# Kernel tuning notes

Measured on AMD Instinct MI355X. Metric: run time of the kernel, lower is better.

The kernel has to match this reference:

```python
import jax, jax.numpy as jnp
import numpy as np
import math

STEM = 64
TOK = 128
RADIUS = 0.16
K = 32


def sinusoidal_pos_emb_3d(x, dim):
    # x: [..., 3] -> [..., dim]; dim/3 channels per axis (half sin, half cos)
    per_axis = dim // 3
    half = per_axis // 2
    scale = math.log(10000.0) / (half - 1)
    freqs = jnp.exp(-scale * jnp.arange(half, dtype=x.dtype))  # [half]
    ang = x[..., :, None] * freqs  # [..., 3, half]
    emb = jnp.concatenate([jnp.sin(ang), jnp.cos(ang)], axis=-1)  # [..., 3, per_axis]
    return emb.reshape(*x.shape[:-1], dim)


def query_ball_point(radius, nsample, xyz):
    # xyz: [B, N, 3] -> idx [B, N, nsample] int32
    B, N, _ = xyz.shape
    d2 = jnp.sum((xyz[:, :, None, :] - xyz[:, None, :, :]) ** 2, axis=-1)  # [B,N,N]
    cand = jnp.where(d2 <= radius * radius, jnp.arange(N, dtype=jnp.int32)[None, None, :], N)
    idx = jnp.sort(cand, axis=-1)[..., :nsample]  # first nsample in-ball indices
    first = idx[..., :1]  # self is always in-ball (d=0), so first is valid
    return jnp.where(idx == N, first, idx)


def index_points(points, idx):
    # points [B,N,C], idx [B,S,K] -> [B,S,K,C]
    return jax.vmap(lambda p, i: p[i])(points, idx)


def point_mlp(x, W, b, activate):
    y = x @ W + b
    return jax.nn.relu(y) if activate else y


def setup_inputs() -> dict:
    key = jax.random.key(0)
    ks = jax.random.split(key, 10)
    B, N = 2, 4096
    xyz = jax.random.uniform(ks[0], (B, N, 3), dtype=jnp.float32)
    point_feature = jax.random.normal(ks[1], (B, N, STEM), dtype=jnp.float32)
    c_in = STEM + 3 + 24 + 96  # 187
    def lin(k, i, o):
        s = 1.0 / np.sqrt(i)
        return jax.random.uniform(k, (i, o), jnp.float32, -s, s)
    W1 = lin(ks[2], c_in, TOK); b1 = jnp.zeros((TOK,), jnp.float32)
    W2 = lin(ks[3], TOK, TOK); b2 = jnp.zeros((TOK,), jnp.float32)
    W3 = lin(ks[4], TOK, TOK); b3 = jnp.zeros((TOK,), jnp.float32)
    W4 = lin(ks[5], TOK, TOK); b4 = jnp.zeros((TOK,), jnp.float32)
    return {"xyz": xyz, "point_feature": point_feature,
            "W1": W1, "b1": b1, "W2": W2, "b2": b2,
            "W3": W3, "b3": b3, "W4": W4, "b4": b4}


def reference(xyz, point_feature, W1, b1, W2, b2, W3, b3, W4, b4):
    idx = query_ball_point(RADIUS, K, xyz)                 # [B,N,K]
    grouped_xyz = index_points(xyz, idx)                   # [B,N,K,3]
    grouped_feature = index_points(point_feature, idx)     # [B,N,K,STEM]
    relative_xyz = grouped_xyz - xyz[:, :, None, :]        # [B,N,K,3]
    rel_pe = sinusoidal_pos_emb_3d(relative_xyz, 24)       # [B,N,K,24]
    abs_pe = sinusoidal_pos_emb_3d(xyz, 96)                # [B,N,96]
    abs_pe = jnp.broadcast_to(abs_pe[:, :, None, :], (*idx.shape, 96))
    grouped_input = jnp.concatenate(
        [grouped_feature, relative_xyz, rel_pe, abs_pe], axis=-1)  # [B,N,K,187]
    h = point_mlp(grouped_input, W1, b1, True)
    h = point_mlp(h, W2, b2, False)                        # [B,N,K,TOK]
    scene_point_feature = jnp.max(h, axis=2)               # [B,N,TOK]
    g = jnp.max(scene_point_feature, axis=1, keepdims=True)  # [B,1,TOK]
    g = point_mlp(g, W3, b3, True)
    return point_mlp(g, W4, b4, False)                     # [B,1,TOK]
```

## Files before the change

### kernel.cpp

```cpp
#include <hip/hip_runtime.h>
#include <stdint.h>

#define BATCH 2
#define NPTS  4096
#define KNBR  32
#define TOKC  128

typedef _Float16 half8 __attribute__((ext_vector_type(8)));
typedef _Float16 half4 __attribute__((ext_vector_type(4)));
typedef float    f32x4 __attribute__((ext_vector_type(4)));

#define OFF_FH    (1u << 20)
#define OFF_AH    (3u << 20)
#define OFF_W1F   ((5u << 20) + 2048)
#define OFF_W2F   ((5u << 20) + 10240)
#define OFF_BMAX  (6u << 20)
#define OFF_BMAX2 (7u << 20)

#define NMAIN 1024

__global__ __launch_bounds__(256) void k_pre(const float* __restrict__ xyz,
                                             const float* __restrict__ feat,
                                             const float* __restrict__ W1,
                                             const float* __restrict__ W2,
                                             const float* __restrict__ b1,
                                             int* __restrict__ oidx,
                                             _Float16* __restrict__ Fh,
                                             _Float16* __restrict__ Ah,
                                             _Float16* __restrict__ W1F,
                                             _Float16* __restrict__ W2F) {
    __shared__ __align__(16) _Float16 inL[16][168];
    const int t = threadIdx.x;
    const int w = t >> 6, lane = t & 63;

    if (blockIdx.x < 2048) {
        int wave = blockIdx.x * 4 + w;
        int b = wave >> 12;
        int n = wave & (NPTS - 1);
        const float* xb = xyz + (size_t)b * NPTS * 3;
        float cx = xb[n * 3 + 0], cy = xb[n * 3 + 1], cz = xb[n * 3 + 2];
        const float R2 = 0.0256f;
        int cnt = 0;
        int first = 0;
        int* out = oidx + (size_t)wave * KNBR;
        for (int base = 0; base < NPTS; base += 256) {
            #pragma clang fp contract(off)
            float pxv[4], pyv[4], pzv[4];
            #pragma unroll
            for (int u = 0; u < 4; u++) {
                int j = base + u * 64 + lane;
                pxv[u] = xb[j * 3 + 0];
                pyv[u] = xb[j * 3 + 1];
                pzv[u] = xb[j * 3 + 2];
            }
            #pragma unroll
            for (int u = 0; u < 4; u++) {
                float dx = pxv[u] - cx, dy = pyv[u] - cy, dz = pzv[u] - cz;
                float d2 = (dx * dx + dy * dy) + dz * dz;
                bool hit = d2 <= R2;
                unsigned long long m = __ballot(hit);
                if (cnt == 0 && m) first = base + u * 64 + (int)__builtin_ctzll(m);
                if (hit) {
                    int pos = cnt + (int)__popcll(m & ((1ull << lane) - 1ull));
                    if (pos < KNBR) out[pos] = base + u * 64 + lane;
                }
                cnt += (int)__popcll(m);
            }
            if (cnt >= KNBR) break;
        }
        if (lane >= cnt && lane < KNBR) out[lane] = first;
        return;
    }

    if (blockIdx.x >= 2560) {
        int f = blockIdx.x - 2560;
        #pragma unroll
        for (int s = 0; s < 2; s++) {
            int e = t + s * 256;
            int ln = e >> 3, j = e & 7;
            int l15 = ln & 15, g = ln >> 4;
            if (f < 8) {
                int k = g * 8 + j;
                int c = f * 16 + l15;
                float val = (k < 27) ? W1[(64 + k) * TOKC + c] : 0.f;
                W1F[f * 512 + e] = (_Float16)val;
            } else {
                int f2 = f - 8;
                int ct = f2 >> 2, kc = f2 & 3;
                int k = kc * 32 + g * 8 + j;
                int c = ct * 16 + l15;
                W2F[f2 * 512 + e] = (_Float16)W2[k * TOKC + c];
            }
        }
        return;
    }

    const int l15 = lane & 15, g = lane >> 4;
    const int g0 = (blockIdx.x - 2048) * 16;

    half8 af[2][2];
    half8 ap[2][3];
    float4 b1v[2];
    #pragma unroll
    for (int rt = 0; rt < 2; rt++) {
        int c = 32 * w + 16 * rt + l15;
        #pragma unroll
        for (int kc = 0; kc < 2; kc++)
            #pragma unroll
            for (int j = 0; j < 8; j++)
                af[rt][kc][j] = (_Float16)W1[(kc * 32 + g * 8 + j) * TOKC + c];
        #pragma unroll
        for (int kc = 0; kc < 3; kc++)
            #pragma unroll
            for (int j = 0; j < 8; j++)
                ap[rt][kc][j] = (_Float16)W1[(91 + kc * 32 + g * 8 + j) * TOKC + c];
        b1v[rt] = *(const float4*)&b1[32 * w + 16 * rt + g * 4];
    }

    {
        float4 v = ((const float4*)(feat + (size_t)g0 * 64))[t];
        half4 hv = {(_Float16)v.x, (_Float16)v.y, (_Float16)v.z, (_Float16)v.w};
        *(half4*)&inL[t >> 4][(t & 15) * 4] = hv;
    }
    {
        int p = t >> 4, v0 = (t & 15) * 6;
        const float* xp = xyz + (size_t)(g0 + p) * 3;
        #pragma unroll
        for (int u = 0; u < 6; u++) {
            int d = v0 + u;
            int a = d >> 5, i = d & 31, fi = i & 15;
            float fr = __expf(-0.6140226914650789f * (float)fi);
            float ang = xp[a] * fr;
            inL[p][64 + d] = (_Float16)((i < 16) ? __sinf(ang) : __cosf(ang));
        }
    }
    __syncthreads();

    f32x4 cF[2], cA[2];
    #pragma unroll
    for (int rt = 0; rt < 2; rt++) { f32x4 z = {0.f, 0.f, 0.f, 0.f}; cF[rt] = z; cA[rt] = z; }
    #pragma unroll
    for (int kc = 0; kc < 2; kc++) {
        half8 bx = *(const half8*)&inL[l15][kc * 32 + g * 8];
        cF[0] = __builtin_amdgcn_mfma_f32_16x16x32_f16(af[0][kc], bx, cF[0], 0, 0, 0);
        cF[1] = __builtin_amdgcn_mfma_f32_16x16x32_f16(af[1][kc], bx, cF[1], 0, 0, 0);
    }
    #pragma unroll
    for (int kc = 0; kc < 3; kc++) {
        half8 bx = *(const half8*)&inL[l15][64 + kc * 32 + g * 8];
        cA[0] = __builtin_amdgcn_mfma_f32_16x16x32_f16(ap[0][kc], bx, cA[0], 0, 0, 0);
        cA[1] = __builtin_amdgcn_mfma_f32_16x16x32_f16(ap[1][kc], bx, cA[1], 0, 0, 0);
    }

    size_t pbase = ((size_t)g0 + l15) * TOKC;
    #pragma unroll
    for (int rt = 0; rt < 2; rt++) {
        int ch0 = 32 * w + 16 * rt + g * 4;
        half4 fv, av;
        #pragma unroll
        for (int r = 0; r < 4; r++) {
            fv[r] = (_Float16)cF[rt][r];
            av[r] = (_Float16)(cA[rt][r] + b1v[rt][r]);
        }
        *(half4*)&Fh[pbase + ch0] = fv;
        *(half4*)&Ah[pbase + ch0] = av;
    }
}

__global__ __launch_bounds__(256, 3) void k_main(const float* __restrict__ xyz,
                                                 const int* __restrict__ idxw,
                                                 const _Float16* __restrict__ Fh,
                                                 const _Float16* __restrict__ Ah,
                                                 const _Float16* __restrict__ W1F,
                                                 const _Float16* __restrict__ W2F,
                                                 float* __restrict__ bmax) {
    __shared__ __align__(16) _Float16 xinL[64 * 40];
    __shared__ __align__(16) _Float16 hfa[64 * 136];
    __shared__ __align__(16) _Float16 arowL[256];
    __shared__ int jidxL[64];

    const int t = threadIdx.x;
    const int w = t >> 6, lane = t & 63;
    const int l15 = lane & 15, g = lane >> 4;
    const int b = blockIdx.x >> 9;
    const int pbase = (blockIdx.x & 511) * 8;
    const float* xb = xyz + (size_t)b * NPTS * 3;

    half8 a1[2];
    half8 a2[2][4];
    #pragma unroll
    for (int rt = 0; rt < 2; rt++) {
        a1[rt] = *(const half8*)&W1F[(2 * w + rt) * 512 + lane * 8];
        #pragma unroll
        for (int kc = 0; kc < 4; kc++)
            a2[rt][kc] = *(const half8*)&W2F[((2 * w + rt) * 4 + kc) * 512 + lane * 8];
    }

    float mxAll[2][4];
    #pragma unroll
    for (int rt = 0; rt < 2; rt++)
        #pragma unroll
        for (int r = 0; r < 4; r++) mxAll[rt][r] = -1e30f;

    const float FR[4] = {1.f, 0.0464158883f, 0.00215443469f, 1e-4f};

    int jreg = 0;
    ushort ar0;
    {
        const size_t gq = (size_t)b * NPTS + pbase;
        if (t < 64) jreg = idxw[gq * KNBR + t];
        ar0 = ((const ushort*)(Ah + gq * TOKC))[t];
    }

    for (int it = 0; it < 4; it++) {
        const int n0 = pbase + it * 2;
        const size_t gp0 = (size_t)b * NPTS + n0;

        if (t < 64) jidxL[t] = jreg;
        ((ushort*)arowL)[t] = ar0;
        __syncthreads();

        if (it < 3) {
            const size_t gq = gp0 + 2;
            if (t < 64) jreg = idxw[gq * KNBR + t];
            ar0 = ((const ushort*)(Ah + gq * TOKC))[t];
        }

        {
            int p = t >> 2, q = t & 3;
            int j = jidxL[p];
            const half8* frp = (const half8*)(Fh + ((size_t)b * NPTS + j) * TOKC + q * 32);
            half8 fb[4];
            #pragma unroll
            for (int i = 0; i < 4; i++) fb[i] = frp[i];
            const half8* arp = (const half8*)(arowL + (p >> 5) * TOKC + q * 32);
            half8* dst = (half8*)(hfa + p * 136 + q * 32);
            #pragma unroll
            for (int i = 0; i < 4; i++) dst[i] = fb[i] + arp[i];
        }
        if (t < 128) {
            int p = t >> 1, hh = t & 1;
            int n = n0 + (p >> 5), j = jidxL[p];
            float rx = xb[j * 3 + 0] - xb[n * 3 + 0];
            float ry = xb[j * 3 + 1] - xb[n * 3 + 1];
            float rz = xb[j * 3 + 2] - xb[n * 3 + 2];
            float v[16];
            if (hh == 0) {
                v[0] = rx; v[1] = ry; v[2] = rz;
                #pragma unroll
                for (int fi = 0; fi < 4; fi++) {
                    float ang = rx * FR[fi];
                    v[3 + fi] = __sinf(ang);
                    v[7 + fi] = __cosf(ang);
                }
                #pragma unroll
                for (int fi = 0; fi < 4; fi++) v[11 + fi] = __sinf(ry * FR[fi]);
                v[15] = __cosf(ry * FR[0]);
            } else {
                #pragma unroll
                for (int fi = 1; fi < 4; fi++) v[fi - 1] = __cosf(ry * FR[fi]);
                #pragma unroll
                for (int fi = 0; fi < 4; fi++) {
                    float ang = rz * FR[fi];
                    v[3 + fi] = __sinf(ang);
                    v[7 + fi] = __cosf(ang);
                }
                #pragma unroll
                for (int i = 11; i < 16; i++) v[i] = 0.f;
            }
            half8 h0, h1;
            #pragma unroll
            for (int i = 0; i < 8; i++) { h0[i] = (_Float16)v[i]; h1[i] = (_Float16)v[8 + i]; }
            *(half8*)&xinL[p * 40 + hh * 16]     = h0;
            *(half8*)&xinL[p * 40 + hh * 16 + 8] = h1;
        }
        __syncthreads();

        #pragma unroll
        for (int ct = 0; ct < 4; ct++) {
            int p = ct * 16 + l15;
            half8 bx = *(const half8*)&xinL[p * 40 + g * 8];
            f32x4 z = {0.f, 0.f, 0.f, 0.f};
            f32x4 c1a = __builtin_amdgcn_mfma_f32_16x16x32_f16(a1[0], bx, z, 0, 0, 0);
            f32x4 c1b = __builtin_amdgcn_mfma_f32_16x16x32_f16(a1[1], bx, z, 0, 0, 0);
            #pragma unroll
            for (int rt = 0; rt < 2; rt++) {
                int ch0 = 32 * w + 16 * rt + g * 4;
                half4* hp = (half4*)&hfa[p * 136 + ch0];
                half4 bias = *hp;
                f32x4 cc = rt ? c1b : c1a;
                half4 hv;
                #pragma unroll
                for (int r = 0; r < 4; r++) {
                    float s = cc[r] + (float)bias[r];
                    hv[r] = (_Float16)fmaxf(s, 0.f);
                }
                *hp = hv;
            }
        }
        __syncthreads();

        f32x4 c2[4][2];
        #pragma unroll
        for (int ct = 0; ct < 4; ct++)
            #pragma unroll
            for (int rt = 0; rt < 2; rt++) {
                f32x4 z = {0.f, 0.f, 0.f, 0.f};
                c2[ct][rt] = z;
            }
        #pragma unroll
        for (int kc = 0; kc < 4; kc++) {
            #pragma unroll
            for (int ct = 0; ct < 4; ct++) {
                half8 bx = *(const half8*)&hfa[(ct * 16 + l15) * 136 + kc * 32 + g * 8];
                c2[ct][0] = __builtin_amdgcn_mfma_f32_16x16x32_f16(a2[0][kc], bx, c2[ct][0], 0, 0, 0);
                c2[ct][1] = __builtin_amdgcn_mfma_f32_16x16x32_f16(a2[1][kc], bx, c2[ct][1], 0, 0, 0);
            }
        }
        #pragma unroll
        for (int rt = 0; rt < 2; rt++)
            #pragma unroll
            for (int r = 0; r < 4; r++) {
                float m0 = fmaxf(fmaxf(c2[0][rt][r], c2[1][rt][r]), fmaxf(c2[2][rt][r], c2[3][rt][r]));
                mxAll[rt][r] = fmaxf(mxAll[rt][r], m0);
            }
        __syncthreads();
    }

    #pragma unroll
    for (int rt = 0; rt < 2; rt++)
        #pragma unroll
        for (int r = 0; r < 4; r++)
            #pragma unroll
            for (int off = 1; off < 16; off <<= 1)
                mxAll[rt][r] = fmaxf(mxAll[rt][r], __shfl_xor(mxAll[rt][r], off));

    if (l15 == 0) {
        float* brow = bmax + (size_t)blockIdx.x * TOKC;
        float4 v0 = make_float4(mxAll[0][0], mxAll[0][1], mxAll[0][2], mxAll[0][3]);
        float4 v1 = make_float4(mxAll[1][0], mxAll[1][1], mxAll[1][2], mxAll[1][3]);
        *(float4*)&brow[32 * w + g * 4]      = v0;
        *(float4*)&brow[32 * w + 16 + g * 4] = v1;
    }
}

__global__ __launch_bounds__(256) void k_red(const float* __restrict__ bmax,
                                             float* __restrict__ bmax2) {
    __shared__ float red[256];
    const int i = blockIdx.x, t = threadIdx.x;
    const int c = t & 127, h = t >> 7;
    const float* base = bmax + ((size_t)i * 16 + (size_t)h * 8) * TOKC + c;
    float m = -1e30f;
    #pragma unroll
    for (int k = 0; k < 8; k++) m = fmaxf(m, base[(size_t)k * TOKC]);
    red[t] = m;
    __syncthreads();
    if (t < 128) bmax2[(size_t)i * TOKC + t] = fmaxf(red[t], red[t + 128]);
}

__global__ __launch_bounds__(256) void k_tail(const float* __restrict__ bmax2,
                                              const float* __restrict__ b2,
                                              const float* __restrict__ W3,
                                              const float* __restrict__ b3,
                                              const float* __restrict__ W4,
                                              const float* __restrict__ b4,
                                              float* __restrict__ out) {
    __shared__ float red[256];
    __shared__ float gl[128], sl[128];
    const int b = blockIdx.x, t = threadIdx.x;
    const int c = t & 127, h = t >> 7;
    const float* base = bmax2 + ((size_t)b * 32 + (size_t)h * 16) * TOKC + c;
    float m = -1e30f;
    #pragma unroll
    for (int k = 0; k < 16; k++) m = fmaxf(m, base[(size_t)k * TOKC]);
    red[t] = m;
    __syncthreads();
    if (t < 128) gl[t] = fmaxf(red[t], red[t + 128]) + b2[t];
    __syncthreads();
    if (t < 128) {
        float s = b3[t];
        for (int k = 0; k < 128; k++) s += gl[k] * W3[k * TOKC + t];
        sl[t] = fmaxf(s, 0.f);
    }
    __syncthreads();
    if (t < 128) {
        float o = b4[t];
        for (int k = 0; k < 128; k++) o += sl[k] * W4[k * TOKC + t];
        out[b * TOKC + t] = o;
    }
}

extern "C" void kernel_launch(void* const* d_in, const int* in_sizes, int n_in,
                              void* d_out, int out_size, void* d_ws, size_t ws_size,
                              hipStream_t stream) {
    const float* xyz  = (const float*)d_in[0];
    const float* feat = (const float*)d_in[1];
    const float* W1   = (const float*)d_in[2];
    const float* b1   = (const float*)d_in[3];
    const float* W2   = (const float*)d_in[4];
    const float* b2   = (const float*)d_in[5];
    const float* W3   = (const float*)d_in[6];
    const float* b3   = (const float*)d_in[7];
    const float* W4   = (const float*)d_in[8];
    const float* b4   = (const float*)d_in[9];

    char* ws = (char*)d_ws;
    int*          idxw  = (int*)ws;
    _Float16*     Fh    = (_Float16*)(ws + OFF_FH);
    _Float16*     Ah    = (_Float16*)(ws + OFF_AH);
    _Float16*     W1F   = (_Float16*)(ws + OFF_W1F);
    _Float16*     W2F   = (_Float16*)(ws + OFF_W2F);
    float*        bmax  = (float*)(ws + OFF_BMAX);
    float*        bmax2 = (float*)(ws + OFF_BMAX2);

    k_pre<<<dim3(2600), dim3(256), 0, stream>>>(xyz, feat, W1, W2, b1,
                                                idxw, Fh, Ah, W1F, W2F);
    k_main<<<dim3(NMAIN), dim3(256), 0, stream>>>(xyz, idxw, Fh, Ah, W1F, W2F, bmax);
    k_red<<<dim3(64), dim3(256), 0, stream>>>(bmax, bmax2);
    k_tail<<<dim3(BATCH), dim3(256), 0, stream>>>(bmax2, b2, W3, b3, W4, b4, (float*)d_out);
}
```

Baseline: 124.5 us.

## Fuse reduction and tail kernels via last-block atomic, prefetch ball-query coords

Merges the two small trailing kernels into one, where the last block to finish (found with an atomic counter reset in the prep kernel) does the final max and the two small MLP layers. This saves one kernel launch and the gap between launches. It also double-buffers the xyz loads in the ball query so the next 256 points are loaded while the current ones are tested. The cost is a threadfence, an atomic counter per call, and more registers in the ball-query path.

```diff
diff --git a/kernel.cpp b/kernel.cpp
--- a/kernel.cpp
+++ b/kernel.cpp
@@ -16,6 +16,7 @@
 #define OFF_W2F   ((5u << 20) + 10240)
 #define OFF_BMAX  (6u << 20)
 #define OFF_BMAX2 (7u << 20)
+#define OFF_CNT   ((7u << 20) + 32768)
 
 #define NMAIN 1024
 
@@ -28,7 +29,8 @@
                                              _Float16* __restrict__ Fh,
                                              _Float16* __restrict__ Ah,
                                              _Float16* __restrict__ W1F,
-                                             _Float16* __restrict__ W2F) {
+                                             _Float16* __restrict__ W2F,
+                                             unsigned int* __restrict__ cntp) {
     __shared__ __align__(16) _Float16 inL[16][168];
     const int t = threadIdx.x;
     const int w = t >> 6, lane = t & 63;
@@ -43,19 +45,28 @@
         int cnt = 0;
         int first = 0;
         int* out = oidx + (size_t)wave * KNBR;
+        float cur[12], nxt[12];
+        #pragma unroll
+        for (int u = 0; u < 4; u++) {
+            int j = u * 64 + lane;
+            cur[u * 3 + 0] = xb[j * 3 + 0];
+            cur[u * 3 + 1] = xb[j * 3 + 1];
+            cur[u * 3 + 2] = xb[j * 3 + 2];
+        }
         for (int base = 0; base < NPTS; base += 256) {
             #pragma clang fp contract(off)
-            float pxv[4], pyv[4], pzv[4];
+            if (base + 256 < NPTS) {
+                #pragma unroll
+                for (int u = 0; u < 4; u++) {
+                    int j = base + 256 + u * 64 + lane;
+                    nxt[u * 3 + 0] = xb[j * 3 + 0];
+                    nxt[u * 3 + 1] = xb[j * 3 + 1];
+                    nxt[u * 3 + 2] = xb[j * 3 + 2];
+                }
+            }
             #pragma unroll
             for (int u = 0; u < 4; u++) {
-                int j = base + u * 64 + lane;
-                pxv[u] = xb[j * 3 + 0];
-                pyv[u] = xb[j * 3 + 1];
-                pzv[u] = xb[j * 3 + 2];
-            }
-            #pragma unroll
-            for (int u = 0; u < 4; u++) {
-                float dx = pxv[u] - cx, dy = pyv[u] - cy, dz = pzv[u] - cz;
+                float dx = cur[u * 3 + 0] - cx, dy = cur[u * 3 + 1] - cy, dz = cur[u * 3 + 2] - cz;
                 float d2 = (dx * dx + dy * dy) + dz * dz;
                 bool hit = d2 <= R2;
                 unsigned long long m = __ballot(hit);
@@ -67,6 +78,8 @@
                 cnt += (int)__popcll(m);
             }
             if (cnt >= KNBR) break;
+            #pragma unroll
+            for (int i = 0; i < 12; i++) cur[i] = nxt[i];
         }
         if (lane >= cnt && lane < KNBR) out[lane] = first;
         return;
@@ -74,6 +87,7 @@
 
     if (blockIdx.x >= 2560) {
         int f = blockIdx.x - 2560;
+        if (f == 0 && t == 0) *cntp = 0u;
         #pragma unroll
         for (int s = 0; s < 2; s++) {
             int e = t + s * 256;
@@ -344,49 +358,57 @@
     }
 }
 
-__global__ __launch_bounds__(256) void k_red(const float* __restrict__ bmax,
-                                             float* __restrict__ bmax2) {
+__global__ __launch_bounds__(256) void k_redtail(const float* __restrict__ bmax,
+                                                 float* __restrict__ bmax2,
+                                                 unsigned int* __restrict__ cntp,
+                                                 const float* __restrict__ b2,
+                                                 const float* __restrict__ W3,
+                                                 const float* __restrict__ b3,
+                                                 const float* __restrict__ W4,
+                                                 const float* __restrict__ b4,
+                                                 float* __restrict__ out) {
     __shared__ float red[256];
+    __shared__ float gl[256], sl[256];
+    __shared__ unsigned int lastFlag;
     const int i = blockIdx.x, t = threadIdx.x;
     const int c = t & 127, h = t >> 7;
-    const float* base = bmax + ((size_t)i * 16 + (size_t)h * 8) * TOKC + c;
-    float m = -1e30f;
-    #pragma unroll
-    for (int k = 0; k < 8; k++) m = fmaxf(m, base[(size_t)k * TOKC]);
-    red[t] = m;
+    {
+        const float* base = bmax + ((size_t)i * 16 + (size_t)h * 8) * TOKC + c;
+        float m = -1e30f;
+        #pragma unroll
+        for (int k = 0; k < 8; k++) m = fmaxf(m, base[(size_t)k * TOKC]);
+        red[t] = m;
+    }
     __syncthreads();
     if (t < 128) bmax2[(size_t)i * TOKC + t] = fmaxf(red[t], red[t + 128]);
-}
-
-__global__ __launch_bounds__(256) void k_tail(const float* __restrict__ bmax2,
-                                              const float* __restrict__ b2,
-                                              const float* __restrict__ W3,
-                                              const float* __restrict__ b3,
-                                              const float* __restrict__ W4,
-                                              const float* __restrict__ b4,
-                                              float* __restrict__ out) {
-    __shared__ float red[256];
-    __shared__ float gl[128], sl[128];
-    const int b = blockIdx.x, t = threadIdx.x;
-    const int c = t & 127, h = t >> 7;
-    const float* base = bmax2 + ((size_t)b * 32 + (size_t)h * 16) * TOKC + c;
-    float m = -1e30f;
-    #pragma unroll
-    for (int k = 0; k < 16; k++) m = fmaxf(m, base[(size_t)k * TOKC]);
-    red[t] = m;
-    __syncthreads();
-    if (t < 128) gl[t] = fmaxf(red[t], red[t + 128]) + b2[t];
-    __syncthreads();
-    if (t < 128) {
-        float s = b3[t];
-        for (int k = 0; k < 128; k++) s += gl[k] * W3[k * TOKC + t];
+    __threadfence();
+    __syncthreads();
+    if (t == 0) lastFlag = (atomicAdd(cntp, 1u) == 63u) ? 1u : 0u;
+    __syncthreads();
+    if (!lastFlag) return;
+
+    const int bb = h;
+    {
+        unsigned int* bp = (unsigned int*)bmax2 + (size_t)bb * 32 * TOKC + c;
+        float m = -1e30f;
+        #pragma unroll
+        for (int k = 0; k < 32; k++) {
+            unsigned int u = atomicOr(&bp[(size_t)k * TOKC], 0u);
+            m = fmaxf(m, __uint_as_float(u));
+        }
+        gl[t] = m + b2[c];
+    }
+    __syncthreads();
+    {
+        float s = b3[c];
+        for (int k = 0; k < 128; k++) s += gl[bb * 128 + k] * W3[k * TOKC + c];
         sl[t] = fmaxf(s, 0.f);
     }
     __syncthreads();
-    if (t < 128) {
-        float o = b4[t];
-        for (int k = 0; k < 128; k++) o += sl[k] * W4[k * TOKC + t];
-        out[b * TOKC + t] = o;
+    {
+        float o = b4[c];
+        for (int k = 0; k < 128; k++) o += sl[bb * 128 + k] * W4[k * TOKC + c];
+        out[t] = o;
     }
 }
 
@@ -412,10 +434,11 @@
     _Float16*     W2F   = (_Float16*)(ws + OFF_W2F);
     float*        bmax  = (float*)(ws + OFF_BMAX);
     float*        bmax2 = (float*)(ws + OFF_BMAX2);
+    unsigned int* cntp  = (unsigned int*)(ws + OFF_CNT);
 
     k_pre<<<dim3(2600), dim3(256), 0, stream>>>(xyz, feat, W1, W2, b1,
-                                                idxw, Fh, Ah, W1F, W2F);
+                                                idxw, Fh, Ah, W1F, W2F, cntp);
     k_main<<<dim3(NMAIN), dim3(256), 0, stream>>>(xyz, idxw, Fh, Ah, W1F, W2F, bmax);
-    k_red<<<dim3(64), dim3(256), 0, stream>>>(bmax, bmax2);
-    k_tail<<<dim3(BATCH), dim3(256), 0, stream>>>(bmax2, b2, W3, b3, W4, b4, (float*)d_out);
+    k_redtail<<<dim3(64), dim3(256), 0, stream>>>(bmax, bmax2, cntp,
+                                                  b2, W3, b3, W4, b4, (float*)d_out);
 }
```

After: 125.4 us. About the same (+0.7%).
